# Performance work log

Measured on AMD Instinct MI355X. Metric: run time of the kernel, lower is better.

The kernel has to match this reference:

```python
import jax, jax.numpy as jnp
import numpy as np

B, S, HID = 2, 2048, 1024
H, KV, D = 8, 4, 128
GROUPS = H // KV
SCALE = D ** -0.5
ROPE_THETA = 10000.0


def _rope_tables(seq_len, dim):
    inv = 1.0 / (ROPE_THETA ** (jnp.arange(0, dim, 2, dtype=jnp.float32) / dim))
    t = jnp.arange(seq_len, dtype=jnp.float32)
    freqs = jnp.outer(t, inv)                          # [S, D/2]
    emb = jnp.concatenate([freqs, freqs], axis=-1)     # [S, D]
    return jnp.cos(emb), jnp.sin(emb)


def _rotate_half(x):
    x1, x2 = jnp.split(x, 2, axis=-1)
    return jnp.concatenate([-x2, x1], axis=-1)


def setup_inputs() -> dict:
    key = jax.random.key(0)
    ks = jax.random.split(key, 7)
    std = 0.02
    hidden = jax.random.normal(ks[0], (B, S, HID), jnp.float32)
    Wq = jax.random.normal(ks[1], (HID, H * D), jnp.float32) * std
    Wk = jax.random.normal(ks[2], (HID, KV * D), jnp.float32) * std
    Wv = jax.random.normal(ks[3], (HID, KV * D), jnp.float32) * std
    Wdt = jax.random.normal(ks[4], (KV * D, H), jnp.float32) * std
    A = jax.random.normal(ks[5], (H,), jnp.float32) * 0.1
    Wo = jax.random.normal(ks[6], (H * D, HID), jnp.float32) * std
    cos, sin = _rope_tables(S, D)
    causal_mask = jnp.triu(jnp.ones((S, S), jnp.int32), 1)[None, None]  # 1 = masked
    return dict(hidden=hidden, Wq=Wq, Wk=Wk, Wv=Wv, Wdt=Wdt, A=A, Wo=Wo,
                cos=cos, sin=sin, causal_mask=causal_mask)


def reference(hidden, Wq, Wk, Wv, Wdt, A, Wo, cos, sin, causal_mask):
    # q/k/v projections -> [B, heads, S, D]
    q = (hidden @ Wq).reshape(B, S, H, D).transpose(0, 2, 1, 3)
    k = (hidden @ Wk).reshape(B, S, KV, D).transpose(0, 2, 1, 3)
    v = (hidden @ Wv).reshape(B, S, KV, D).transpose(0, 2, 1, 3)
    # RoPE
    c = cos[None, None]  # [1,1,S,D]
    s = sin[None, None]
    q = q * c + _rotate_half(q) * s
    k = k * c + _rotate_half(k) * s
    # dynamic mask: dt_proj over flattened per-position value states
    v_flat = v.transpose(0, 2, 1, 3).reshape(B, S, KV * D)
    dt = v_flat @ Wdt                                        # [B, S, H]
    dyn = jnp.exp(A[None, None, :] * jax.nn.softplus(dt))    # [B, S, H]
    attn_bias = dyn.transpose(0, 2, 1)[:, :, None, :]        # [B, H, 1, kv]
    min_val = jnp.finfo(jnp.float32).min
    attn_bias = jnp.where(causal_mask != 0, min_val, attn_bias)  # [B, H, S, S]
    # GQA repeat of kv heads
    k_rep = jnp.repeat(k, GROUPS, axis=1)
    v_rep = jnp.repeat(v, GROUPS, axis=1)
    scores = jnp.einsum('bhqd,bhkd->bhqk', q, k_rep) * SCALE + attn_bias
    w = jax.nn.softmax(scores.astype(jnp.float32), axis=-1).astype(hidden.dtype)
    out = jnp.einsum('bhqk,bhkd->bhqd', w, v_rep)
    out = out.transpose(0, 2, 1, 3).reshape(B, S, H * D)
    return out @ Wo
```

## Files before the change

kernel.cpp:

```cpp
#include <hip/hip_runtime.h>

typedef unsigned short u16;
typedef unsigned int   u32;
typedef __bf16 bf16;
typedef bf16  bf16x8 __attribute__((ext_vector_type(8)));
typedef float f32x4  __attribute__((ext_vector_type(4)));

#define S_LEN 2048
#define SCALE 0.08838834764831845f
#define SMAX  8.0f

__device__ __forceinline__ float bf2f(u16 u) {
  union { u32 i; float f; } v; v.i = ((u32)u) << 16; return v.f;
}
__device__ __forceinline__ u16 f2b(float f) {
  union { float f; u32 i; } v; v.f = f;
  u32 x = v.i;
  u32 r = x + 0x7fffu + ((x >> 16) & 1u);
  return (u16)(r >> 16);
}
__device__ __forceinline__ float2 bfpair(u32 u) {
  union { u32 i; float f; } lo, hi;
  lo.i = u << 16; hi.i = u & 0xffff0000u;
  float2 r; r.x = lo.f; r.y = hi.f; return r;
}

__device__ __forceinline__ void gl_lds16(const u16* g, u16* l) {
  __builtin_amdgcn_global_load_lds(
      (const __attribute__((address_space(1))) void*)g,
      (__attribute__((address_space(3))) void*)l, 16, 0, 0);
}

__device__ __forceinline__ void load16(const float* p, u16* dst) {
  #pragma unroll
  for (int i = 0; i < 16; i += 4) {
    float4 v = *(const float4*)(p + i);
    dst[i]     = f2b(v.x); dst[i + 1] = f2b(v.y);
    dst[i + 2] = f2b(v.z); dst[i + 3] = f2b(v.w);
  }
}

__device__ __forceinline__ void storeo(float* p, float v) { *p = v; }
__device__ __forceinline__ void storeo(u16* p, float v)   { *p = f2b(v); }

__device__ __forceinline__ bf16x8 frag8(const u16* p) {
  union { uint4 u; bf16x8 v; } c;
  c.u = *(const uint4*)p;
  return c.v;
}
__device__ __forceinline__ f32x4 zero4() {
  f32x4 z = {0.f, 0.f, 0.f, 0.f}; return z;
}

__global__ __launch_bounds__(256) void prep_kernel(
    const float* __restrict__ H, u16* __restrict__ HB,
    const float* __restrict__ Wq, const float* __restrict__ Wk,
    const float* __restrict__ Wv, const float* __restrict__ Wo,
    u16* __restrict__ Wqt, u16* __restrict__ Wkt,
    u16* __restrict__ Wvt, u16* __restrict__ Wot)
{
  const int bid = blockIdx.x;
  if (bid < 2048) {
    const size_t base = ((size_t)bid * 256 + threadIdx.x) * 8;
    float4 a = *(const float4*)(H + base);
    float4 b = *(const float4*)(H + base + 4);
    u16 tmp[8];
    tmp[0]=f2b(a.x); tmp[1]=f2b(a.y); tmp[2]=f2b(a.z); tmp[3]=f2b(a.w);
    tmp[4]=f2b(b.x); tmp[5]=f2b(b.y); tmp[6]=f2b(b.z); tmp[7]=f2b(b.w);
    *(uint4*)(HB + base) = *(uint4*)tmp;
    return;
  }
  const int b2 = bid - 2048;
  const float* src; u16* dst; int N, ko, no;
  if (b2 < 256)      { src = Wq; dst = Wqt; N = 1024; int q = b2;       ko = (q >> 4) * 64; no = (q & 15) * 64; }
  else if (b2 < 384) { src = Wk; dst = Wkt; N = 512;  int q = b2 - 256; ko = (q >> 3) * 64; no = (q & 7) * 64; }
  else if (b2 < 512) { src = Wv; dst = Wvt; N = 512;  int q = b2 - 384; ko = (q >> 3) * 64; no = (q & 7) * 64; }
  else               { src = Wo; dst = Wot; N = 1024; int q = b2 - 512; ko = (q >> 4) * 64; no = (q & 15) * 64; }

  __shared__ __align__(16) u16 T[64][68];
  const int t = threadIdx.x;
  const int r = t >> 2, c = (t & 3) * 16;
  {
    u16 tmp[16];
    load16(src + (size_t)(ko + r) * N + no + c, tmp);
    *(uint4*)&T[r][c]     = *(uint4*)tmp;
    *(uint4*)&T[r][c + 8] = *(uint4*)(tmp + 8);
  }
  __syncthreads();
  {
    u16 tmp[16];
    #pragma unroll
    for (int j = 0; j < 16; ++j) tmp[j] = T[c + j][r];
    u16* o = dst + (size_t)(no + r) * 1024 + ko + c;
    *(uint4*)o       = *(uint4*)tmp;
    *(uint4*)(o + 8) = *(uint4*)(tmp + 8);
  }
}

__global__ __launch_bounds__(256) void gemm3(
    const u16* __restrict__ A, int lda, int Kdim,
    const u16* __restrict__ W0, u16* __restrict__ O0, int ldo0,
    const u16* __restrict__ W1, u16* __restrict__ O1, int ldo1,
    const u16* __restrict__ W2, u16* __restrict__ O2, int ldo2,
    int c1, int c2,
    const float* __restrict__ cosb, const float* __restrict__ sinb, int ropeLim,
    u16* __restrict__ VTg)
{
  const int flat = blockIdx.y * gridDim.x + blockIdx.x;
  const int xcd = flat & 7, rr = flat >> 3;
  const int bx = ((xcd & 1) << 3) + (rr & 7);
  const int by = ((xcd >> 1) << 3) + (rr >> 3);
  const int n0 = bx * 128;
  const int m0 = by * 128;
  const u16* W; u16* O; int ldo, col;
  if (n0 < c1)      { W = W0; O = O0; ldo = ldo0; col = n0; }
  else if (n0 < c2) { W = W1; O = O1; ldo = ldo1; col = n0 - c1; }
  else              { W = W2; O = O2; ldo = ldo2; col = n0 - c2; }
  const bool doRope = (n0 < ropeLim);
  const bool isV    = (n0 >= c2);

  __shared__ __align__(16) u16 As[2][128 * 64];
  __shared__ __align__(16) u16 Bs[2][128 * 64];

  const int t    = threadIdx.x;
  const int w    = t >> 6, lane = t & 63, quad = lane >> 4, l16 = lane & 15;
  const int sw   = l16 & 7;
  const int srow = lane >> 3;
  const int schk = (lane & 7) ^ srow;
  int kcs[2];
  #pragma unroll
  for (int ks = 0; ks < 2; ++ks) kcs[ks] = ((ks * 4 + quad) ^ sw) * 8;

  const u16* Ag = A + (size_t)(m0 + w * 32 + srow) * lda + schk * 8;
  const u16* Bg = W + (size_t)(col + w * 32 + srow) * Kdim + schk * 8;

  f32x4 acc[2][8];
  #pragma unroll
  for (int i2 = 0; i2 < 2; ++i2)
    #pragma unroll
    for (int nt = 0; nt < 8; ++nt) acc[i2][nt] = zero4();

  #pragma unroll
  for (int j = 0; j < 4; ++j) {
    gl_lds16(Ag + (size_t)(j * 8) * lda, &As[0][(w * 4 + j) * 512]);
    gl_lds16(Bg + (size_t)(j * 8) * Kdim, &Bs[0][(w * 4 + j) * 512]);
  }

  int cur = 0;
  for (int k0 = 0; k0 < Kdim; k0 += 64, cur ^= 1) {
    __syncthreads();
    if (k0 + 64 < Kdim) {
      #pragma unroll
      for (int j = 0; j < 4; ++j) {
        gl_lds16(Ag + (size_t)(j * 8) * lda + k0 + 64, &As[cur ^ 1][(w * 4 + j) * 512]);
        gl_lds16(Bg + (size_t)(j * 8) * Kdim + k0 + 64, &Bs[cur ^ 1][(w * 4 + j) * 512]);
      }
    }
    #pragma unroll
    for (int ks = 0; ks < 2; ++ks) {
      bf16x8 a0 = frag8(&As[cur][(w * 32 + l16) * 64 + kcs[ks]]);
      bf16x8 a1 = frag8(&As[cur][(w * 32 + 16 + l16) * 64 + kcs[ks]]);
      #pragma unroll
      for (int nt = 0; nt < 8; ++nt) {
        bf16x8 bw = frag8(&Bs[cur][(nt * 16 + l16) * 64 + kcs[ks]]);
        acc[0][nt] = __builtin_amdgcn_mfma_f32_16x16x32_bf16(a0, bw, acc[0][nt], 0, 0, 0);
        acc[1][nt] = __builtin_amdgcn_mfma_f32_16x16x32_bf16(a1, bw, acc[1][nt], 0, 0, 0);
      }
    }
  }

  if (doRope) {
    #pragma unroll
    for (int i2 = 0; i2 < 2; ++i2)
      #pragma unroll
      for (int r = 0; r < 4; ++r) {
        const int m = m0 + w * 32 + i2 * 16 + quad * 4 + r;
        const int sp_ = m & (S_LEN - 1);
        const float* cp = cosb + (size_t)sp_ * 128;
        const float* sp = sinb + (size_t)sp_ * 128;
        #pragma unroll
        for (int nt = 0; nt < 4; ++nt) {
          const int d = nt * 16 + l16;
          const float a  = acc[i2][nt][r];
          const float bb = acc[i2][nt + 4][r];
          acc[i2][nt][r]     = a * cp[d]       - bb * sp[d];
          acc[i2][nt + 4][r] = bb * cp[d + 64] + a * sp[d + 64];
        }
      }
  }

  #pragma unroll
  for (int i2 = 0; i2 < 2; ++i2)
    #pragma unroll
    for (int nt = 0; nt < 8; ++nt)
      #pragma unroll
      for (int r = 0; r < 4; ++r) {
        const int m = m0 + w * 32 + i2 * 16 + quad * 4 + r;
        const int n = col + nt * 16 + l16;
        O[(size_t)m * ldo + n] = f2b(acc[i2][nt][r]);
      }

  if (isV) {
    #pragma unroll
    for (int i2 = 0; i2 < 2; ++i2)
      #pragma unroll
      for (int nt = 0; nt < 8; ++nt) {
        const int m = m0 + w * 32 + i2 * 16 + quad * 4;
        const int bb_ = m >> 11, ss = m & (S_LEN - 1);
        const int d = col + nt * 16 + l16;
        u16 tmp4[4];
        #pragma unroll
        for (int r = 0; r < 4; ++r) tmp4[r] = f2b(acc[i2][nt][r]);
        u16* dst = VTg + ((size_t)((bb_ * 4 + (d >> 7)) * 128 + (d & 127))) * S_LEN + ss;
        *(uint2*)dst = *(const uint2*)tmp4;
      }
  }
}

template <typename TO>
__global__ __launch_bounds__(256) void gemm2(
    const u16* __restrict__ A, int lda, int Kdim,
    const u16* __restrict__ W0, TO* __restrict__ O0, int ldo0,
    const u16* __restrict__ W1, TO* __restrict__ O1, int ldo1,
    const u16* __restrict__ W2, TO* __restrict__ O2, int ldo2,
    int c1, int c2)
{
  const int flat = blockIdx.y * gridDim.x + blockIdx.x;
  const int xcd = flat & 7, rr = flat >> 3;
  const int bx = ((xcd & 1) << 3) + (rr & 7);
  const int by = ((xcd >> 1) << 3) + (rr >> 3);
  const int n0 = bx * 64;
  const int m0 = by * 128;
  const u16* W; TO* O; int ldo, col;
  if (n0 < c1)      { W = W0; O = O0; ldo = ldo0; col = n0; }
  else if (n0 < c2) { W = W1; O = O1; ldo = ldo1; col = n0 - c1; }
  else              { W = W2; O = O2; ldo = ldo2; col = n0 - c2; }

  __shared__ __align__(16) u16 As[2][128 * 64];
  __shared__ __align__(16) u16 Bs[2][64 * 64];

  const int t    = threadIdx.x;
  const int w    = t >> 6, lane = t & 63, quad = lane >> 4, l16 = lane & 15;
  const int sw   = l16 & 7;
  const int srow = lane >> 3;
  const int schk = (lane & 7) ^ srow;
  int kcs[2];
  #pragma unroll
  for (int ks = 0; ks < 2; ++ks) kcs[ks] = ((ks * 4 + quad) ^ sw) * 8;

  const u16* Ag = A + (size_t)(m0 + w * 32 + srow) * lda + schk * 8;
  const u16* Bg = W + (size_t)(col + w * 16 + srow) * Kdim + schk * 8;

  f32x4 acc[2][4];
  #pragma unroll
  for (int i2 = 0; i2 < 2; ++i2)
    #pragma unroll
    for (int nt = 0; nt < 4; ++nt) acc[i2][nt] = zero4();

  #pragma unroll
  for (int j = 0; j < 4; ++j)
    gl_lds16(Ag + (size_t)(j * 8) * lda, &As[0][(w * 4 + j) * 512]);
  #pragma unroll
  for (int j = 0; j < 2; ++j)
    gl_lds16(Bg + (size_t)(j * 8) * Kdim, &Bs[0][(w * 2 + j) * 512]);

  int cur = 0;
  for (int k0 = 0; k0 < Kdim; k0 += 64, cur ^= 1) {
    __syncthreads();
    if (k0 + 64 < Kdim) {
      #pragma unroll
      for (int j = 0; j < 4; ++j)
        gl_lds16(Ag + (size_t)(j * 8) * lda + k0 + 64, &As[cur ^ 1][(w * 4 + j) * 512]);
      #pragma unroll
      for (int j = 0; j < 2; ++j)
        gl_lds16(Bg + (size_t)(j * 8) * Kdim + k0 + 64, &Bs[cur ^ 1][(w * 2 + j) * 512]);
    }
    #pragma unroll
    for (int ks = 0; ks < 2; ++ks) {
      bf16x8 a0 = frag8(&As[cur][(w * 32 + l16) * 64 + kcs[ks]]);
      bf16x8 a1 = frag8(&As[cur][(w * 32 + 16 + l16) * 64 + kcs[ks]]);
      #pragma unroll
      for (int nt = 0; nt < 4; ++nt) {
        bf16x8 bw = frag8(&Bs[cur][(nt * 16 + l16) * 64 + kcs[ks]]);
        acc[0][nt] = __builtin_amdgcn_mfma_f32_16x16x32_bf16(a0, bw, acc[0][nt], 0, 0, 0);
        acc[1][nt] = __builtin_amdgcn_mfma_f32_16x16x32_bf16(a1, bw, acc[1][nt], 0, 0, 0);
      }
    }
  }
  #pragma unroll
  for (int i2 = 0; i2 < 2; ++i2)
    #pragma unroll
    for (int nt = 0; nt < 4; ++nt)
      #pragma unroll
      for (int r = 0; r < 4; ++r) {
        const int m = m0 + w * 32 + i2 * 16 + quad * 4 + r;
        const int n = col + nt * 16 + l16;
        storeo(O + (size_t)m * ldo + n, acc[i2][nt][r]);
      }
}

__global__ __launch_bounds__(256) void dyn_kernel(const u16* __restrict__ Vb, const float* __restrict__ Wdt,
                                                  const float* __restrict__ Af, float* __restrict__ dynT)
{
  __shared__ __align__(16) float Wl[4096];
  const int t = threadIdx.x;
  #pragma unroll
  for (int i = 0; i < 4; ++i)
    *(float4*)&Wl[(t + i * 256) * 4] = *(const float4*)(Wdt + (t + i * 256) * 4);
  __syncthreads();

  const int wid = t >> 6, lane = t & 63;
  const int pos = blockIdx.x * 4 + wid;
  float acc[8];
  #pragma unroll
  for (int h = 0; h < 8; ++h) acc[h] = 0.f;
  for (int j = lane; j < 512; j += 64) {
    float v = bf2f(Vb[(size_t)pos * 512 + j]);
    float4 w0 = *(const float4*)&Wl[j * 8];
    float4 w1 = *(const float4*)&Wl[j * 8 + 4];
    acc[0] += v * w0.x; acc[1] += v * w0.y; acc[2] += v * w0.z; acc[3] += v * w0.w;
    acc[4] += v * w1.x; acc[5] += v * w1.y; acc[6] += v * w1.z; acc[7] += v * w1.w;
  }
  #pragma unroll
  for (int off = 32; off > 0; off >>= 1)
    #pragma unroll
    for (int h = 0; h < 8; ++h) acc[h] += __shfl_down(acc[h], off, 64);
  if (lane == 0) {
    const int b = pos >> 11, s = pos & (S_LEN - 1);
    #pragma unroll
    for (int h = 0; h < 8; ++h) {
      float dt = acc[h];
      float sp = (dt > 20.f) ? dt : log1pf(__expf(dt));
      dynT[(size_t)(b * 8 + h) * S_LEN + s] = __expf(Af[h] * sp);
    }
  }
}

__global__ __launch_bounds__(256, 3) void attn_mfma(const u16* __restrict__ Qb, const u16* __restrict__ Kb,
                                                    const u16* __restrict__ VTg, const float* __restrict__ dynT,
                                                    u16* __restrict__ ctx,
                                                    u16* __restrict__ PO, float* __restrict__ PL)
{
  const int idx = blockIdx.x;
  const int g = (idx & 7) | (((idx >> 3) & 1) << 3);
  const int b = g >> 3, h = g & 7, kvh = h >> 1;
  const int fp = 79 - (idx >> 4);
  int s, c;
  if (fp < 8)       { s = fp; c = 0; }
  else if (fp < 24) { s = 8 + ((fp - 8) >> 1);  c = (fp - 8) & 1; }
  else if (fp < 48) { int r2 = fp - 24; int q3 = r2 / 3; s = 16 + q3; c = r2 - q3 * 3; }
  else              { s = 24 + ((fp - 48) >> 2); c = (fp - 48) & 3; }
  const int q0  = s * 64;
  const int kt0 = c * 8;
  const int kt1 = (c == (s >> 3)) ? s : (kt0 + 7);

  __shared__ __align__(16) u16 Ks[64 * 128];
  __shared__ __align__(16) u16 Vs[128 * 64];
  __shared__ __align__(16) u16 Ps[4][16 * 64];

  const int t = threadIdx.x;
  const int wid = t >> 6, lane = t & 63, quad = lane >> 4, l16 = lane & 15;
  const int sw = l16 & 7;

  int kcs[4], pcs[2];
  #pragma unroll
  for (int ks = 0; ks < 4; ++ks) kcs[ks] = ((ks * 4 + quad) ^ sw) * 8;
  const int phr = sw ^ ((l16 >> 3) << 1);
  #pragma unroll
  for (int ks = 0; ks < 2; ++ks) pcs[ks] = ((ks * 4 + quad) ^ phr) * 8;

  const u16* KgL[4];
  const u16* VgL[4];
  #pragma unroll
  for (int j = 0; j < 4; ++j) {
    const int krj = (wid * 4 + j) * 4 + (lane >> 4);
    const int kcj = (lane & 15) ^ (((j & 1) << 2) + (lane >> 4));
    KgL[j] = Kb + (size_t)(b * S_LEN + krj) * 512 + kvh * 128 + kcj * 8;
    const int vrj = (wid * 4 + j) * 8 + (lane >> 3);
    const int vcj = (lane & 7) ^ (lane >> 3);
    VgL[j] = VTg + ((size_t)((b * 4 + kvh) * 128 + vrj)) * S_LEN + vcj * 8;
  }

  bf16x8 qf[4];
  {
    const u16* qrow = Qb + (size_t)(b * S_LEN + q0 + wid * 16 + l16) * 1024 + h * 128 + quad * 8;
    #pragma unroll
    for (int ks = 0; ks < 4; ++ks) qf[ks] = frag8(qrow + ks * 32);
  }

  const float* dynbase = dynT + (size_t)(b * 8 + h) * S_LEN + l16;

  f32x4 accO[8];
  #pragma unroll
  for (int nt = 0; nt < 8; ++nt) accO[nt] = zero4();
  float l_lane[4] = {0.f, 0.f, 0.f, 0.f};

  for (int kt = kt0; kt <= kt1; ++kt) {
    const int k0 = kt * 64;
    __syncthreads();
    #pragma unroll
    for (int j = 0; j < 4; ++j)
      gl_lds16(KgL[j] + (size_t)k0 * 512, &Ks[(wid * 4 + j) * 512]);
    #pragma unroll
    for (int j = 0; j < 4; ++j)
      gl_lds16(VgL[j] + k0, &Vs[(wid * 4 + j) * 512]);
    float dv[4];
    #pragma unroll
    for (int nt = 0; nt < 4; ++nt) dv[nt] = dynbase[k0 + nt * 16];
    __syncthreads();

    f32x4 accS[4];
    #pragma unroll
    for (int nt = 0; nt < 4; ++nt) accS[nt] = zero4();
    __builtin_amdgcn_s_setprio(1);
    #pragma unroll
    for (int ks = 0; ks < 4; ++ks)
      #pragma unroll
      for (int nt = 0; nt < 4; ++nt)
        accS[nt] = __builtin_amdgcn_mfma_f32_16x16x32_bf16(
            qf[ks], frag8(&Ks[(nt * 16 + l16) * 128 + kcs[ks]]), accS[nt], 0, 0, 0);
    __builtin_amdgcn_s_setprio(0);

    if (kt < s) {
      #pragma unroll
      for (int nt = 0; nt < 4; ++nt)
        #pragma unroll
        for (int r = 0; r < 4; ++r) {
          float p = __expf(fmaf(accS[nt][r], SCALE, dv[nt]) - SMAX);
          l_lane[r] += p;
          const int prow = quad * 4 + r;
          const int ph = (prow & 7) ^ ((prow >> 3) << 1);
          Ps[wid][prow * 64 + (((nt * 2 + (l16 >> 3)) ^ ph) << 3) + sw] = f2b(p);
        }
    } else {
      const int qq = wid * 16 + quad * 4;
      #pragma unroll
      for (int nt = 0; nt < 4; ++nt) {
        const int kk = nt * 16 + l16;
        #pragma unroll
        for (int r = 0; r < 4; ++r) {
          float p = (kk > qq + r) ? 0.f
                    : __expf(fmaf(accS[nt][r], SCALE, dv[nt]) - SMAX);
          l_lane[r] += p;
          const int prow = quad * 4 + r;
          const int ph = (prow & 7) ^ ((prow >> 3) << 1);
          Ps[wid][prow * 64 + (((nt * 2 + (l16 >> 3)) ^ ph) << 3) + sw] = f2b(p);
        }
      }
    }

    __builtin_amdgcn_s_setprio(1);
    #pragma unroll
    for (int ks = 0; ks < 2; ++ks) {
      bf16x8 a = frag8(&Ps[wid][l16 * 64 + pcs[ks]]);
      #pragma unroll
      for (int nt = 0; nt < 8; ++nt)
        accO[nt] = __builtin_amdgcn_mfma_f32_16x16x32_bf16(
            a, frag8(&Vs[(nt * 16 + l16) * 64 + kcs[ks]]), accO[nt], 0, 0, 0);
    }
    __builtin_amdgcn_s_setprio(0);
  }

  #pragma unroll
  for (int off = 1; off < 16; off <<= 1)
    #pragma unroll
    for (int r = 0; r < 4; ++r) l_lane[r] += __shfl_xor(l_lane[r], off, 64);

  if (s < 8) {
    float linv[4];
    #pragma unroll
    for (int r = 0; r < 4; ++r) linv[r] = 1.f / l_lane[r];
    #pragma unroll
    for (int nt = 0; nt < 8; ++nt)
      #pragma unroll
      for (int r = 0; r < 4; ++r) {
        const int qq = q0 + wid * 16 + quad * 4 + r;
        const int d  = nt * 16 + l16;
        ctx[(size_t)(b * S_LEN + qq) * 1024 + h * 128 + d] = f2b(accO[nt][r] * linv[r]);
      }
  } else {
    const int slot = g * 72 + (fp - 8);
    u16 tmp[32];
    #pragma unroll
    for (int nt = 0; nt < 8; ++nt)
      #pragma unroll
      for (int r = 0; r < 4; ++r) tmp[nt * 4 + r] = f2b(accO[nt][r]);
    u16* po = PO + (size_t)slot * 8192 + wid * 2048 + lane * 32;
    #pragma unroll
    for (int i = 0; i < 4; ++i) *(uint4*)(po + i * 8) = *(uint4*)(tmp + i * 8);
    if (l16 == 0) {
      #pragma unroll
      for (int r = 0; r < 4; ++r) PL[slot * 64 + wid * 16 + quad * 4 + r] = l_lane[r];
    }
  }
}

__global__ __launch_bounds__(256) void attn_combine(const u16* __restrict__ PO, const float* __restrict__ PL,
                                                    u16* __restrict__ ctx)
{
  const int s = 8 + (int)blockIdx.x;
  const int g = (int)blockIdx.y;
  const int b = g >> 3, h = g & 7;
  const int g2 = s >> 3;
  const int nch = g2 + 1;
  const int base = (g2 == 1) ? 8 : (g2 == 2) ? 24 : 48;
  const int slot0 = g * 72 + base + (s - g2 * 8) * nch - 8;
  const int t = threadIdx.x;
  const int wid = t >> 6, lane = t & 63, quad = lane >> 4, l16 = lane & 15;

  float acc[32];
  #pragma unroll
  for (int i = 0; i < 32; ++i) acc[i] = 0.f;
  float ls[4] = {0.f, 0.f, 0.f, 0.f};

  for (int cth = 0; cth < nch; ++cth) {
    const u16* po = PO + (size_t)(slot0 + cth) * 8192 + wid * 2048 + lane * 32;
    #pragma unroll
    for (int i = 0; i < 4; ++i) {
      uint4 v = *(const uint4*)(po + i * 8);
      u32 u[4] = {v.x, v.y, v.z, v.w};
      #pragma unroll
      for (int j = 0; j < 4; ++j) {
        float2 p = bfpair(u[j]);
        acc[i * 8 + 2 * j]     += p.x;
        acc[i * 8 + 2 * j + 1] += p.y;
      }
    }
    #pragma unroll
    for (int r = 0; r < 4; ++r) ls[r] += PL[(slot0 + cth) * 64 + wid * 16 + quad * 4 + r];
  }

  float linv[4];
  #pragma unroll
  for (int r = 0; r < 4; ++r) linv[r] = 1.f / ls[r];
  #pragma unroll
  for (int nt = 0; nt < 8; ++nt)
    #pragma unroll
    for (int r = 0; r < 4; ++r) {
      const int qq = s * 64 + wid * 16 + quad * 4 + r;
      const int d  = nt * 16 + l16;
      ctx[(size_t)(b * S_LEN + qq) * 1024 + h * 128 + d] = f2b(acc[nt * 4 + r] * linv[r]);
    }
}

extern "C" void kernel_launch(void* const* d_in, const int* in_sizes, int n_in,
                              void* d_out, int out_size, void* d_ws, size_t ws_size,
                              hipStream_t stream)
{
  const float* hidden = (const float*)d_in[0];
  const float* Wq     = (const float*)d_in[1];
  const float* Wk     = (const float*)d_in[2];
  const float* Wv     = (const float*)d_in[3];
  const float* Wdt    = (const float*)d_in[4];
  const float* Af     = (const float*)d_in[5];
  const float* Wo     = (const float*)d_in[6];
  const float* cosb   = (const float*)d_in[7];
  const float* sinb   = (const float*)d_in[8];
  float* out = (float*)d_out;

  u16* Qb  = (u16*)d_ws;
  u16* Kb  = Qb + (size_t)4096 * 1024;
  u16* Vb  = Kb + (size_t)4096 * 512;
  u16* VTg = Vb + (size_t)4096 * 512;
  float* dynT = (float*)(VTg + (size_t)4096 * 512);
  u16* PO = (u16*)(dynT + (size_t)16 * S_LEN);
  float* PL = (float*)(PO + (size_t)16 * 72 * 8192);
  u16* HB  = (u16*)(PL + (size_t)16 * 72 * 64);
  u16* Wqt = HB  + (size_t)4096 * 1024;
  u16* Wkt = Wqt + (size_t)1024 * 1024;
  u16* Wvt = Wkt + (size_t)512 * 1024;
  u16* Wot = Wvt + (size_t)512 * 1024;
  u16* ctx = Qb;

  prep_kernel<<<2816, 256, 0, stream>>>(hidden, HB, Wq, Wk, Wv, Wo, Wqt, Wkt, Wvt, Wot);
  gemm3<<<dim3(16, 32), 256, 0, stream>>>(HB, 1024, 1024,
      Wqt, Qb, 1024,
      Wkt, Kb,  512,
      Wvt, Vb,  512,
      1024, 1536,
      cosb, sinb, 1536, VTg);
  dyn_kernel<<<1024, 256, 0, stream>>>(Vb, Wdt, Af, dynT);
  attn_mfma<<<1280, 256, 0, stream>>>(Qb, Kb, VTg, dynT, ctx, PO, PL);
  attn_combine<<<dim3(24, 16), 256, 0, stream>>>(PO, PL, ctx);
  gemm2<float><<<dim3(16, 32), 256, 0, stream>>>(ctx, 1024, 1024,
      Wot, out, 1024,
      Wot, out, 1024,
      Wot, out, 1024,
      1 << 30, 1 << 30);
}
```

Before: 206.5 us.

## Use 128-wide KV tiles and simpler two-way split-K attention scheduling

The attention kernel now processes 128 keys per iteration instead of 64, which doubles the K/V shared-memory tiles and the P buffer. The split-K work assignment is rebuilt so query tiles past the midpoint are split into at most two chunks, and the partial-output slots and combine kernel shrink to match. The goal is fewer barriers and loop iterations per key, more MFMA work per load, and fewer blocks and combine reads. In exchange it uses more LDS and registers, drops the launch-bounds occupancy hint from 3 to 2, and makes load balance across blocks coarser.

```diff
diff --git a/kernel.cpp b/kernel.cpp
--- a/kernel.cpp
+++ b/kernel.cpp
@@ -336,7 +336,7 @@
   }
 }
 
-__global__ __launch_bounds__(256, 3) void attn_mfma(const u16* __restrict__ Qb, const u16* __restrict__ Kb,
+__global__ __launch_bounds__(256, 2) void attn_mfma(const u16* __restrict__ Qb, const u16* __restrict__ Kb,
                                                     const u16* __restrict__ VTg, const float* __restrict__ dynT,
                                                     u16* __restrict__ ctx,
                                                     u16* __restrict__ PO, float* __restrict__ PL)
@@ -344,41 +344,35 @@
   const int idx = blockIdx.x;
   const int g = (idx & 7) | (((idx >> 3) & 1) << 3);
   const int b = g >> 3, h = g & 7, kvh = h >> 1;
-  const int fp = 79 - (idx >> 4);
-  int s, c;
-  if (fp < 8)       { s = fp; c = 0; }
-  else if (fp < 24) { s = 8 + ((fp - 8) >> 1);  c = (fp - 8) & 1; }
-  else if (fp < 48) { int r2 = fp - 24; int q3 = r2 / 3; s = 16 + q3; c = r2 - q3 * 3; }
-  else              { s = 24 + ((fp - 48) >> 2); c = (fp - 48) & 3; }
-  const int q0  = s * 64;
-  const int kt0 = c * 8;
-  const int kt1 = (c == (s >> 3)) ? s : (kt0 + 7);
-
-  __shared__ __align__(16) u16 Ks[64 * 128];
-  __shared__ __align__(16) u16 Vs[128 * 64];
-  __shared__ __align__(16) u16 Ps[4][16 * 64];
+  const int f = idx >> 4;
+  int s, c, kt0, kt1;
+  if (f < 16)      { s = 16 + f; c = 0; kt0 = 0; kt1 = 7; }
+  else if (f < 32) { s = 47 - f; c = 1; kt0 = 8; kt1 = s >> 1; }
+  else             { s = 47 - f; c = 0; kt0 = 0; kt1 = s >> 1; }
+  const int q0 = s * 64;
+  const int dt = s >> 1;
+
+  __shared__ __align__(16) u16 Ks[128 * 128];
+  __shared__ __align__(16) u16 Vs[128 * 128];
+  __shared__ __align__(16) u16 Ps[4][16 * 128];
 
   const int t = threadIdx.x;
   const int wid = t >> 6, lane = t & 63, quad = lane >> 4, l16 = lane & 15;
-  const int sw = l16 & 7;
-
-  int kcs[4], pcs[2];
+  const int sw = l16 & 7, hi = l16 >> 3;
+
+  int kcs[4];
   #pragma unroll
   for (int ks = 0; ks < 4; ++ks) kcs[ks] = ((ks * 4 + quad) ^ sw) * 8;
-  const int phr = sw ^ ((l16 >> 3) << 1);
-  #pragma unroll
-  for (int ks = 0; ks < 2; ++ks) pcs[ks] = ((ks * 4 + quad) ^ phr) * 8;
-
-  const u16* KgL[4];
-  const u16* VgL[4];
-  #pragma unroll
-  for (int j = 0; j < 4; ++j) {
-    const int krj = (wid * 4 + j) * 4 + (lane >> 4);
-    const int kcj = (lane & 15) ^ (((j & 1) << 2) + (lane >> 4));
-    KgL[j] = Kb + (size_t)(b * S_LEN + krj) * 512 + kvh * 128 + kcj * 8;
-    const int vrj = (wid * 4 + j) * 8 + (lane >> 3);
-    const int vcj = (lane & 7) ^ (lane >> 3);
-    VgL[j] = VTg + ((size_t)((b * 4 + kvh) * 128 + vrj)) * S_LEN + vcj * 8;
+
+  const u16* KgL[2];
+  const u16* VgL[2];
+  {
+    const int g0 = hi * 8 + (sw ^ quad);
+    const int g1 = hi * 8 + (sw ^ quad ^ 4);
+    KgL[0] = Kb + (size_t)(b * S_LEN + wid * 32 + quad) * 512 + kvh * 128 + g0 * 8;
+    KgL[1] = Kb + (size_t)(b * S_LEN + wid * 32 + 4 + quad) * 512 + kvh * 128 + g1 * 8;
+    VgL[0] = VTg + ((size_t)((b * 4 + kvh) * 128 + wid * 32 + quad)) * S_LEN + g0 * 8;
+    VgL[1] = VTg + ((size_t)((b * 4 + kvh) * 128 + wid * 32 + 4 + quad)) * S_LEN + g1 * 8;
   }
 
   bf16x8 qf[4];
@@ -396,46 +390,45 @@
   float l_lane[4] = {0.f, 0.f, 0.f, 0.f};
 
   for (int kt = kt0; kt <= kt1; ++kt) {
-    const int k0 = kt * 64;
+    const int k0 = kt * 128;
     __syncthreads();
     #pragma unroll
-    for (int j = 0; j < 4; ++j)
-      gl_lds16(KgL[j] + (size_t)k0 * 512, &Ks[(wid * 4 + j) * 512]);
-    #pragma unroll
-    for (int j = 0; j < 4; ++j)
-      gl_lds16(VgL[j] + k0, &Vs[(wid * 4 + j) * 512]);
-    float dv[4];
-    #pragma unroll
-    for (int nt = 0; nt < 4; ++nt) dv[nt] = dynbase[k0 + nt * 16];
+    for (int j = 0; j < 8; ++j)
+      gl_lds16(KgL[j & 1] + (size_t)(k0 + (j >> 1) * 8) * 512, &Ks[(wid * 8 + j) * 512]);
+    #pragma unroll
+    for (int j = 0; j < 8; ++j)
+      gl_lds16(VgL[j & 1] + (size_t)((j >> 1) * 8) * S_LEN + k0, &Vs[(wid * 8 + j) * 512]);
+    float dv[8];
+    #pragma unroll
+    for (int nt = 0; nt < 8; ++nt) dv[nt] = dynbase[k0 + nt * 16];
     __syncthreads();
 
-    f32x4 accS[4];
-    #pragma unroll
-    for (int nt = 0; nt < 4; ++nt) accS[nt] = zero4();
+    f32x4 accS[8];
+    #pragma unroll
+    for (int nt = 0; nt < 8; ++nt) accS[nt] = zero4();
     __builtin_amdgcn_s_setprio(1);
     #pragma unroll
     for (int ks = 0; ks < 4; ++ks)
       #pragma unroll
-      for (int nt = 0; nt < 4; ++nt)
+      for (int nt = 0; nt < 8; ++nt)
         accS[nt] = __builtin_amdgcn_mfma_f32_16x16x32_bf16(
             qf[ks], frag8(&Ks[(nt * 16 + l16) * 128 + kcs[ks]]), accS[nt], 0, 0, 0);
     __builtin_amdgcn_s_setprio(0);
 
-    if (kt < s) {
-      #pragma unroll
-      for (int nt = 0; nt < 4; ++nt)
+    if (kt < dt) {
+      #pragma unroll
+      for (int nt = 0; nt < 8; ++nt)
         #pragma unroll
         for (int r = 0; r < 4; ++r) {
           float p = __expf(fmaf(accS[nt][r], SCALE, dv[nt]) - SMAX);
           l_lane[r] += p;
           const int prow = quad * 4 + r;
-          const int ph = (prow & 7) ^ ((prow >> 3) << 1);
-          Ps[wid][prow * 64 + (((nt * 2 + (l16 >> 3)) ^ ph) << 3) + sw] = f2b(p);
+          Ps[wid][prow * 128 + (((nt * 2 + hi) ^ (prow & 7)) << 3) + sw] = f2b(p);
         }
     } else {
-      const int qq = wid * 16 + quad * 4;
-      #pragma unroll
-      for (int nt = 0; nt < 4; ++nt) {
+      const int qq = (s & 1) * 64 + wid * 16 + quad * 4;
+      #pragma unroll
+      for (int nt = 0; nt < 8; ++nt) {
         const int kk = nt * 16 + l16;
         #pragma unroll
         for (int r = 0; r < 4; ++r) {
@@ -443,20 +436,19 @@
                     : __expf(fmaf(accS[nt][r], SCALE, dv[nt]) - SMAX);
           l_lane[r] += p;
           const int prow = quad * 4 + r;
-          const int ph = (prow & 7) ^ ((prow >> 3) << 1);
-          Ps[wid][prow * 64 + (((nt * 2 + (l16 >> 3)) ^ ph) << 3) + sw] = f2b(p);
+          Ps[wid][prow * 128 + (((nt * 2 + hi) ^ (prow & 7)) << 3) + sw] = f2b(p);
         }
       }
     }
 
     __builtin_amdgcn_s_setprio(1);
     #pragma unroll
-    for (int ks = 0; ks < 2; ++ks) {
-      bf16x8 a = frag8(&Ps[wid][l16 * 64 + pcs[ks]]);
+    for (int ks = 0; ks < 4; ++ks) {
+      bf16x8 a = frag8(&Ps[wid][l16 * 128 + kcs[ks]]);
       #pragma unroll
       for (int nt = 0; nt < 8; ++nt)
         accO[nt] = __builtin_amdgcn_mfma_f32_16x16x32_bf16(
-            a, frag8(&Vs[(nt * 16 + l16) * 64 + kcs[ks]]), accO[nt], 0, 0, 0);
+            a, frag8(&Vs[(nt * 16 + l16) * 128 + kcs[ks]]), accO[nt], 0, 0, 0);
     }
     __builtin_amdgcn_s_setprio(0);
   }
@@ -466,7 +458,7 @@
     #pragma unroll
     for (int r = 0; r < 4; ++r) l_lane[r] += __shfl_xor(l_lane[r], off, 64);
 
-  if (s < 8) {
+  if (s < 16) {
     float linv[4];
     #pragma unroll
     for (int r = 0; r < 4; ++r) linv[r] = 1.f / l_lane[r];
@@ -479,7 +471,7 @@
         ctx[(size_t)(b * S_LEN + qq) * 1024 + h * 128 + d] = f2b(accO[nt][r] * linv[r]);
       }
   } else {
-    const int slot = g * 72 + (fp - 8);
+    const int slot = g * 32 + (s - 16) * 2 + c;
     u16 tmp[32];
     #pragma unroll
     for (int nt = 0; nt < 8; ++nt)
@@ -498,13 +490,11 @@
 __global__ __launch_bounds__(256) void attn_combine(const u16* __restrict__ PO, const float* __restrict__ PL,
                                                     u16* __restrict__ ctx)
 {
-  const int s = 8 + (int)blockIdx.x;
+  const int sx = (int)blockIdx.x;
+  const int s = 16 + sx;
   const int g = (int)blockIdx.y;
   const int b = g >> 3, h = g & 7;
-  const int g2 = s >> 3;
-  const int nch = g2 + 1;
-  const int base = (g2 == 1) ? 8 : (g2 == 2) ? 24 : 48;
-  const int slot0 = g * 72 + base + (s - g2 * 8) * nch - 8;
+  const int slot0 = g * 32 + sx * 2;
   const int t = threadIdx.x;
   const int wid = t >> 6, lane = t & 63, quad = lane >> 4, l16 = lane & 15;
 
@@ -513,7 +503,8 @@
   for (int i = 0; i < 32; ++i) acc[i] = 0.f;
   float ls[4] = {0.f, 0.f, 0.f, 0.f};
 
-  for (int cth = 0; cth < nch; ++cth) {
+  #pragma unroll
+  for (int cth = 0; cth < 2; ++cth) {
     const u16* po = PO + (size_t)(slot0 + cth) * 8192 + wid * 2048 + lane * 32;
     #pragma unroll
     for (int i = 0; i < 4; ++i) {
@@ -564,8 +555,8 @@
   u16* VTg = Vb + (size_t)4096 * 512;
   float* dynT = (float*)(VTg + (size_t)4096 * 512);
   u16* PO = (u16*)(dynT + (size_t)16 * S_LEN);
-  float* PL = (float*)(PO + (size_t)16 * 72 * 8192);
-  u16* HB  = (u16*)(PL + (size_t)16 * 72 * 64);
+  float* PL = (float*)(PO + (size_t)16 * 32 * 8192);
+  u16* HB  = (u16*)(PL + (size_t)16 * 32 * 64);
   u16* Wqt = HB  + (size_t)4096 * 1024;
   u16* Wkt = Wqt + (size_t)1024 * 1024;
   u16* Wvt = Wkt + (size_t)512 * 1024;
@@ -580,8 +571,8 @@
       1024, 1536,
       cosb, sinb, 1536, VTg);
   dyn_kernel<<<1024, 256, 0, stream>>>(Vb, Wdt, Af, dynT);
-  attn_mfma<<<1280, 256, 0, stream>>>(Qb, Kb, VTg, dynT, ctx, PO, PL);
-  attn_combine<<<dim3(24, 16), 256, 0, stream>>>(PO, PL, ctx);
+  attn_mfma<<<768, 256, 0, stream>>>(Qb, Kb, VTg, dynT, ctx, PO, PL);
+  attn_combine<<<dim3(16, 16), 256, 0, stream>>>(PO, PL, ctx);
   gemm2<float><<<dim3(16, 32), 256, 0, stream>>>(ctx, 1024, 1024,
       Wot, out, 1024,
       Wot, out, 1024,
```

Result: faster. 201.1 us (-2.7%).
